# Kernel optimization log

Measured on AMD Instinct MI355X. Metric: run time of the kernel, lower is better.

## Reference

```python
import jax, jax.numpy as jnp
import numpy as np

# Deformable Aggregation (DAF) core of Sparse4DHead1st:
# multi-camera, multi-level bilinear point sampling + grouped weighted reduction.
# feature:            [bs, num_cams, sum(H_l*W_l), C]
# spatial_shapes:     [num_levels, 2] (H, W) per level (static metadata)
# level_start_index:  [num_levels] offsets into the flattened HW axis
# points_2d:          [bs, num_anchor, num_pts, num_cams, 2] normalized (x, y) in [0, 1]
# weights:            [bs, num_anchor, num_pts, num_cams, num_levels, num_groups]
# output:             [bs, num_anchor, C]  (sum over pts, cams, levels)

BS, CAMS, C = 1, 6, 256
NUM_ANCHOR, NUM_PTS = 900, 13
NUM_LEVELS, NUM_GROUPS = 4, 8
LEVEL_SHAPES = np.array([[64, 176], [32, 88], [16, 44], [8, 22]], np.int32)


def setup_inputs() -> dict:
    key = jax.random.key(0)
    k1, k2, k3 = jax.random.split(key, 3)
    hw = LEVEL_SHAPES[:, 0] * LEVEL_SHAPES[:, 1]
    starts = np.concatenate([[0], np.cumsum(hw)[:-1]]).astype(np.int32)
    total = int(hw.sum())  # 14960
    feature = jax.random.normal(k1, (BS, CAMS, total, C), jnp.float32)
    points_2d = jax.random.uniform(k2, (BS, NUM_ANCHOR, NUM_PTS, CAMS, 2), jnp.float32)
    # learned attention weights (normalized-ish so outputs stay O(1))
    weights = jax.random.uniform(
        k3, (BS, NUM_ANCHOR, NUM_PTS, CAMS, NUM_LEVELS, NUM_GROUPS), jnp.float32
    ) / (NUM_PTS * CAMS * NUM_LEVELS)
    return {
        "feature": feature,
        "spatial_shapes": jnp.asarray(LEVEL_SHAPES),
        "level_start_index": jnp.asarray(starts),
        "points_2d": points_2d,
        "weights": weights,
    }


def reference(feature, spatial_shapes, level_start_index, points_2d, weights):
    # spatial shapes / starts are static metadata (control slicing sizes)
    shapes = np.asarray(spatial_shapes)
    starts = np.asarray(level_start_index)
    bs, cams, _, c = feature.shape
    _, A, P, _, _ = points_2d.shape
    L, G = weights.shape[-2], weights.shape[-1]
    gc = c // G  # channels per group
    rowids = jnp.arange(bs * cams)[:, None]

    px = points_2d[..., 0]  # [bs, A, P, cams], normalized x
    py = points_2d[..., 1]

    out = jnp.zeros((bs, A, G, gc), feature.dtype)
    for l in range(L):
        h, w = int(shapes[l, 0]), int(shapes[l, 1])
        s = int(starts[l])
        feat = feature[:, :, s : s + h * w, :].reshape(bs * cams, h * w, c)
        x = px * w - 0.5
        y = py * h - 0.5
        x0 = jnp.floor(x)
        y0 = jnp.floor(y)
        bil = 0.0
        for dx in (0, 1):
            for dy in (0, 1):
                xi = x0 + dx
                yi = y0 + dy
                cw = (1.0 - jnp.abs(x - xi)) * (1.0 - jnp.abs(y - yi))
                valid = (xi >= 0) & (xi < w) & (yi >= 0) & (yi < h)
                idx = (jnp.clip(yi, 0, h - 1) * w + jnp.clip(xi, 0, w - 1)).astype(jnp.int32)
                # [bs, A, P, cams] -> [bs*cams, A*P]
                idx = idx.transpose(0, 3, 1, 2).reshape(bs * cams, A * P)
                cwm = (cw * valid).transpose(0, 3, 1, 2).reshape(bs * cams, A * P)
                v = feat[rowids, idx]  # gather: [bs*cams, A*P, C]
                bil = bil + v * cwm[..., None]
        bil = bil.reshape(bs, cams, A, P, G, gc)
        out = out + jnp.einsum("bcapgd,bapcg->bagd", bil, weights[..., l, :])
    return out.reshape(bs, A, c)
```

## Files before the change

### kernel.cpp

```cpp
#include <hip/hip_runtime.h>

#define NA 900
#define NP 13
#define NCAM 6
#define NL 4
#define NG 8
#define NC 256
#define TOTALHW 14960
#define NPC (NP * NCAM)
#define NS (NPC * NL)
#define NW 8
#define FEAT_ELEMS (NCAM * TOTALHW * NC)

__device__ __constant__ int c_h[NL]  = {64, 32, 16, 8};
__device__ __constant__ int c_w[NL]  = {176, 88, 44, 22};
__device__ __constant__ int c_st[NL] = {0, 11264, 14080, 14784};

__device__ __forceinline__ float bfu(unsigned short u) {
    union { unsigned int i; float f; } x;
    x.i = ((unsigned int)u) << 16;
    return x.f;
}

__global__ __launch_bounds__(256) void cvt_kernel(
    const float* __restrict__ src, unsigned short* __restrict__ dst)
{
    const int n4 = FEAT_ELEMS / 4;
    for (int i = blockIdx.x * 256 + threadIdx.x; i < n4; i += gridDim.x * 256) {
        const float4 v = ((const float4*)src)[i];
        ushort4 o;
        const float* pv = (const float*)&v;
        unsigned short* po = (unsigned short*)&o;
        #pragma unroll
        for (int k = 0; k < 4; ++k) {
            union { float f; unsigned int u; } x;
            x.f = pv[k];
            unsigned int r = x.u + 0x7FFFu + ((x.u >> 16) & 1u);
            po[k] = (unsigned short)(r >> 16);
        }
        ((ushort4*)dst)[i] = o;
    }
}

__global__ __launch_bounds__(512) void daf_bf16_kernel(
    const unsigned short* __restrict__ featb,
    const float* __restrict__ points,
    const float* __restrict__ weights,
    float* __restrict__ out)
{
    const int a    = blockIdx.x;
    const int tid  = threadIdx.x;
    const int wv   = tid >> 6;
    const int lane = tid & 63;

    __shared__ int    s_idx[NS][4];
    __shared__ float  s_cw[NS][4];
    __shared__ float  s_wg[NS * NG];
    __shared__ float4 s_part[NW][64];

    const float* wsrc = weights + (size_t)a * NS * NG;
    for (int i = tid; i < NS * NG; i += 512) {
        const int g  = i & (NG - 1);
        const int s  = i >> 3;
        const int l  = s / NPC;
        const int pc = s - l * NPC;
        s_wg[i] = wsrc[(pc * NL + l) * NG + g];
    }

    if (tid < NS) {
        const int s   = tid;
        const int l   = s / NPC;
        const int pc  = s - l * NPC;
        const int cam = pc % NCAM;
        const int p   = pc / NCAM;

        const float2 pt = *(const float2*)(points + (((size_t)a * NP + p) * NCAM + cam) * 2);
        const int h  = c_h[l];
        const int w  = c_w[l];
        const int st = c_st[l];

        const float x   = pt.x * (float)w - 0.5f;
        const float y   = pt.y * (float)h - 0.5f;
        const float x0f = floorf(x);
        const float y0f = floorf(y);
        const int   x0  = (int)x0f;
        const int   y0  = (int)y0f;
        const float fx  = x - x0f;
        const float fy  = y - y0f;
        const float wx[2] = {1.0f - fx, fx};
        const float wy[2] = {1.0f - fy, fy};

        const int base = cam * TOTALHW + st;
        #pragma unroll
        for (int k = 0; k < 4; ++k) {
            const int dx = k & 1;
            const int dy = k >> 1;
            const int xi = x0 + dx;
            const int yi = y0 + dy;
            const bool valid = (xi >= 0) && (xi < w) && (yi >= 0) && (yi < h);
            const int xc = min(max(xi, 0), w - 1);
            const int yc = min(max(yi, 0), h - 1);
            s_idx[s][k] = base + yc * w + xc;
            s_cw[s][k]  = valid ? wx[dx] * wy[dy] : 0.0f;
        }
    }
    __syncthreads();

    const int g = lane >> 3;
    const ushort4* __restrict__ fb = (const ushort4*)featb;

    float4 acc = make_float4(0.f, 0.f, 0.f, 0.f);
    #pragma unroll 2
    for (int s = wv; s < NS; s += NW) {
        const float wg = s_wg[s * NG + g];
        const int   i0 = s_idx[s][0], i1 = s_idx[s][1], i2 = s_idx[s][2], i3 = s_idx[s][3];
        const float c0 = s_cw[s][0] * wg, c1 = s_cw[s][1] * wg;
        const float c2 = s_cw[s][2] * wg, c3 = s_cw[s][3] * wg;

        const ushort4 r0 = fb[(size_t)i0 * 64 + lane];
        const ushort4 r1 = fb[(size_t)i1 * 64 + lane];
        const ushort4 r2 = fb[(size_t)i2 * 64 + lane];
        const ushort4 r3 = fb[(size_t)i3 * 64 + lane];

        acc.x += bfu(r0.x) * c0 + bfu(r1.x) * c1 + bfu(r2.x) * c2 + bfu(r3.x) * c3;
        acc.y += bfu(r0.y) * c0 + bfu(r1.y) * c1 + bfu(r2.y) * c2 + bfu(r3.y) * c3;
        acc.z += bfu(r0.z) * c0 + bfu(r1.z) * c1 + bfu(r2.z) * c2 + bfu(r3.z) * c3;
        acc.w += bfu(r0.w) * c0 + bfu(r1.w) * c1 + bfu(r2.w) * c2 + bfu(r3.w) * c3;
    }

    s_part[wv][lane] = acc;
    __syncthreads();

    if (tid < 64) {
        float4 r = s_part[0][lane];
        #pragma unroll
        for (int k = 1; k < NW; ++k) {
            const float4 p = s_part[k][lane];
            r.x += p.x; r.y += p.y; r.z += p.z; r.w += p.w;
        }
        ((float4*)out)[(size_t)a * 64 + lane] = r;
    }
}

__global__ __launch_bounds__(512) void daf_f32_kernel(
    const float* __restrict__ feature,
    const float* __restrict__ points,
    const float* __restrict__ weights,
    float* __restrict__ out)
{
    const int a    = blockIdx.x;
    const int tid  = threadIdx.x;
    const int wv   = tid >> 6;
    const int lane = tid & 63;

    __shared__ int    s_idx[NS][4];
    __shared__ float  s_cw[NS][4];
    __shared__ float  s_wg[NS * NG];
    __shared__ float4 s_part[NW][64];

    const float* wsrc = weights + (size_t)a * NS * NG;
    for (int i = tid; i < NS * NG; i += 512) {
        const int g  = i & (NG - 1);
        const int s  = i >> 3;
        const int l  = s / NPC;
        const int pc = s - l * NPC;
        s_wg[i] = wsrc[(pc * NL + l) * NG + g];
    }

    if (tid < NS) {
        const int s   = tid;
        const int l   = s / NPC;
        const int pc  = s - l * NPC;
        const int cam = pc % NCAM;
        const int p   = pc / NCAM;

        const float2 pt = *(const float2*)(points + (((size_t)a * NP + p) * NCAM + cam) * 2);
        const int h  = c_h[l];
        const int w  = c_w[l];
        const int st = c_st[l];

        const float x   = pt.x * (float)w - 0.5f;
        const float y   = pt.y * (float)h - 0.5f;
        const float x0f = floorf(x);
        const float y0f = floorf(y);
        const int   x0  = (int)x0f;
        const int   y0  = (int)y0f;
        const float fx  = x - x0f;
        const float fy  = y - y0f;
        const float wx[2] = {1.0f - fx, fx};
        const float wy[2] = {1.0f - fy, fy};

        const int base = cam * TOTALHW + st;
        #pragma unroll
        for (int k = 0; k < 4; ++k) {
            const int dx = k & 1;
            const int dy = k >> 1;
            const int xi = x0 + dx;
            const int yi = y0 + dy;
            const bool valid = (xi >= 0) && (xi < w) && (yi >= 0) && (yi < h);
            const int xc = min(max(xi, 0), w - 1);
            const int yc = min(max(yi, 0), h - 1);
            s_idx[s][k] = base + yc * w + xc;
            s_cw[s][k]  = valid ? wx[dx] * wy[dy] : 0.0f;
        }
    }
    __syncthreads();

    const int g = lane >> 3;
    const float4* __restrict__ f4 = (const float4*)feature;

    float4 acc = make_float4(0.f, 0.f, 0.f, 0.f);
    for (int s = wv; s < NS; s += NW) {
        const float wg = s_wg[s * NG + g];
        const int   i0 = s_idx[s][0], i1 = s_idx[s][1], i2 = s_idx[s][2], i3 = s_idx[s][3];
        const float c0 = s_cw[s][0] * wg, c1 = s_cw[s][1] * wg;
        const float c2 = s_cw[s][2] * wg, c3 = s_cw[s][3] * wg;

        const float4 v0 = f4[(size_t)i0 * 64 + lane];
        const float4 v1 = f4[(size_t)i1 * 64 + lane];
        const float4 v2 = f4[(size_t)i2 * 64 + lane];
        const float4 v3 = f4[(size_t)i3 * 64 + lane];

        acc.x += v0.x * c0 + v1.x * c1 + v2.x * c2 + v3.x * c3;
        acc.y += v0.y * c0 + v1.y * c1 + v2.y * c2 + v3.y * c3;
        acc.z += v0.z * c0 + v1.z * c1 + v2.z * c2 + v3.z * c3;
        acc.w += v0.w * c0 + v1.w * c1 + v2.w * c2 + v3.w * c3;
    }

    s_part[wv][lane] = acc;
    __syncthreads();

    if (tid < 64) {
        float4 r = s_part[0][lane];
        #pragma unroll
        for (int k = 1; k < NW; ++k) {
            const float4 p = s_part[k][lane];
            r.x += p.x; r.y += p.y; r.z += p.z; r.w += p.w;
        }
        ((float4*)out)[(size_t)a * 64 + lane] = r;
    }
}

extern "C" void kernel_launch(void* const* d_in, const int* in_sizes, int n_in,
                              void* d_out, int out_size, void* d_ws, size_t ws_size,
                              hipStream_t stream) {
    const float* feature        = (const float*)d_in[0];
    const float* points         = (const float*)d_in[3];
    const float* weights        = (const float*)d_in[4];
    float*       out            = (float*)d_out;

    const size_t need = (size_t)FEAT_ELEMS * sizeof(unsigned short);
    if (ws_size >= need && d_ws != nullptr) {
        unsigned short* featb = (unsigned short*)d_ws;
        cvt_kernel<<<2048, 256, 0, stream>>>(feature, featb);
        daf_bf16_kernel<<<NA, 512, 0, stream>>>(featb, points, weights, out);
    } else {
        daf_f32_kernel<<<NA, 512, 0, stream>>>(feature, points, weights, out);
    }
}
```

Before: 204.2 us.

## Split DAF into per-level kernels with software-pipelined gathers and wider bf16 conversion

Replaces the single fused bf16 sampling kernel with four launches, one per pyramid level, each templated on its level shape. Each launch accumulates into the output, and the coarsest level initialises it. Inside each launch the gather loop is software-pipelined: the next sample's four feature rows are prefetched while the current one is accumulated. The conversion kernel now handles eight floats per thread with 16-byte stores. The per-level split is meant to keep one level's feature working set resident in cache, at the cost of three extra launches and read-modify-write traffic on the output.

New measurement: 214.9 us. 1.05x slower.

```diff
diff --git a/kernel.cpp b/kernel.cpp
--- a/kernel.cpp
+++ b/kernel.cpp
@@ -7,14 +7,9 @@
 #define NG 8
 #define NC 256
 #define TOTALHW 14960
-#define NPC (NP * NCAM)
-#define NS (NPC * NL)
 #define NW 8
+#define NSL (NP * NCAM)
 #define FEAT_ELEMS (NCAM * TOTALHW * NC)
-
-__device__ __constant__ int c_h[NL]  = {64, 32, 16, 8};
-__device__ __constant__ int c_w[NL]  = {176, 88, 44, 22};
-__device__ __constant__ int c_st[NL] = {0, 11264, 14080, 14784};
 
 __device__ __forceinline__ float bfu(unsigned short u) {
     union { unsigned int i; float f; } x;
@@ -23,27 +18,162 @@
 }
 
 __global__ __launch_bounds__(256) void cvt_kernel(
-    const float* __restrict__ src, unsigned short* __restrict__ dst)
+    const uint4* __restrict__ src, uint4* __restrict__ dst)
 {
-    const int n4 = FEAT_ELEMS / 4;
-    for (int i = blockIdx.x * 256 + threadIdx.x; i < n4; i += gridDim.x * 256) {
-        const float4 v = ((const float4*)src)[i];
-        ushort4 o;
-        const float* pv = (const float*)&v;
-        unsigned short* po = (unsigned short*)&o;
+    const int n8 = FEAT_ELEMS / 8;
+    for (int i = blockIdx.x * 256 + threadIdx.x; i < n8; i += gridDim.x * 256) {
+        union { uint4 u; float f[4]; } a, b;
+        a.u = src[2 * i];
+        b.u = src[2 * i + 1];
+        unsigned int w[8];
         #pragma unroll
         for (int k = 0; k < 4; ++k) {
             union { float f; unsigned int u; } x;
-            x.f = pv[k];
-            unsigned int r = x.u + 0x7FFFu + ((x.u >> 16) & 1u);
-            po[k] = (unsigned short)(r >> 16);
-        }
-        ((ushort4*)dst)[i] = o;
-    }
-}
-
-__global__ __launch_bounds__(512) void daf_bf16_kernel(
+            x.f = a.f[k];
+            w[k] = (x.u + 0x7FFFu + ((x.u >> 16) & 1u)) >> 16;
+            x.f = b.f[k];
+            w[4 + k] = (x.u + 0x7FFFu + ((x.u >> 16) & 1u)) >> 16;
+        }
+        uint4 o;
+        o.x = w[0] | (w[1] << 16);
+        o.y = w[2] | (w[3] << 16);
+        o.z = w[4] | (w[5] << 16);
+        o.w = w[6] | (w[7] << 16);
+        dst[i] = o;
+    }
+}
+
+template<int L, int H, int W, int ST, bool INIT>
+__global__ __launch_bounds__(512) void daf_level(
     const unsigned short* __restrict__ featb,
+    const float* __restrict__ points,
+    const float* __restrict__ weights,
+    float* __restrict__ out)
+{
+    const int a    = blockIdx.x;
+    const int tid  = threadIdx.x;
+    const int wv   = tid >> 6;
+    const int lane = tid & 63;
+
+    __shared__ int    s_idx[NSL][4];
+    __shared__ float  s_cw[NSL][4];
+    __shared__ float  s_wg[NSL * NG];
+    __shared__ float4 s_part[NW][64];
+
+    const float* wsrc = weights + (size_t)a * NP * NCAM * NL * NG;
+    for (int i = tid; i < NSL * NG; i += 512) {
+        const int g   = i & (NG - 1);
+        const int s   = i >> 3;
+        const int cam = s / NP;
+        const int p   = s - cam * NP;
+        s_wg[i] = wsrc[((p * NCAM + cam) * NL + L) * NG + g];
+    }
+
+    if (tid < NSL) {
+        const int s   = tid;
+        const int cam = s / NP;
+        const int p   = s - cam * NP;
+
+        const float2 pt = *(const float2*)(points + (((size_t)a * NP + p) * NCAM + cam) * 2);
+        const float x   = pt.x * (float)W - 0.5f;
+        const float y   = pt.y * (float)H - 0.5f;
+        const float x0f = floorf(x);
+        const float y0f = floorf(y);
+        const int   x0  = (int)x0f;
+        const int   y0  = (int)y0f;
+        const float fx  = x - x0f;
+        const float fy  = y - y0f;
+        const float wx[2] = {1.0f - fx, fx};
+        const float wy[2] = {1.0f - fy, fy};
+
+        const int base = cam * TOTALHW + ST;
+        #pragma unroll
+        for (int k = 0; k < 4; ++k) {
+            const int dx = k & 1;
+            const int dy = k >> 1;
+            const int xi = x0 + dx;
+            const int yi = y0 + dy;
+            const bool valid = (xi >= 0) && (xi < W) && (yi >= 0) && (yi < H);
+            const int xc = min(max(xi, 0), W - 1);
+            const int yc = min(max(yi, 0), H - 1);
+            s_idx[s][k] = base + yc * W + xc;
+            s_cw[s][k]  = valid ? wx[dx] * wy[dy] : 0.0f;
+        }
+    }
+    __syncthreads();
+
+    const int g = lane >> 3;
+    const ushort4* __restrict__ fb = (const ushort4*)featb;
+
+    float4 acc = make_float4(0.f, 0.f, 0.f, 0.f);
+
+    int s = wv;
+    int4   ii;  float4 cc;  float wg = 0.f;
+    ushort4 r0, r1, r2, r3;
+    if (s < NSL) {
+        ii = *(const int4*)s_idx[s];
+        cc = *(const float4*)s_cw[s];
+        wg = s_wg[s * NG + g];
+        r0 = fb[(size_t)ii.x * 64 + lane];
+        r1 = fb[(size_t)ii.y * 64 + lane];
+        r2 = fb[(size_t)ii.z * 64 + lane];
+        r3 = fb[(size_t)ii.w * 64 + lane];
+    }
+    while (s < NSL) {
+        const int sn = s + NW;
+        int4 ni; float4 nc; float nwg = 0.f;
+        ushort4 n0, n1, n2, n3;
+        if (sn < NSL) {
+            ni  = *(const int4*)s_idx[sn];
+            nc  = *(const float4*)s_cw[sn];
+            nwg = s_wg[sn * NG + g];
+            n0 = fb[(size_t)ni.x * 64 + lane];
+            n1 = fb[(size_t)ni.y * 64 + lane];
+            n2 = fb[(size_t)ni.z * 64 + lane];
+            n3 = fb[(size_t)ni.w * 64 + lane];
+        }
+        const float c0 = cc.x * wg, c1 = cc.y * wg;
+        const float c2 = cc.z * wg, c3 = cc.w * wg;
+
+        acc.x += bfu(r0.x) * c0 + bfu(r1.x) * c1 + bfu(r2.x) * c2 + bfu(r3.x) * c3;
+        acc.y += bfu(r0.y) * c0 + bfu(r1.y) * c1 + bfu(r2.y) * c2 + bfu(r3.y) * c3;
+        acc.z += bfu(r0.z) * c0 + bfu(r1.z) * c1 + bfu(r2.z) * c2 + bfu(r3.z) * c3;
+        acc.w += bfu(r0.w) * c0 + bfu(r1.w) * c1 + bfu(r2.w) * c2 + bfu(r3.w) * c3;
+
+        r0 = n0; r1 = n1; r2 = n2; r3 = n3;
+        cc = nc; wg = nwg;
+        s = sn;
+    }
+
+    s_part[wv][lane] = acc;
+    __syncthreads();
+
+    if (tid < 64) {
+        float4 r = s_part[0][lane];
+        #pragma unroll
+        for (int k = 1; k < NW; ++k) {
+            const float4 p = s_part[k][lane];
+            r.x += p.x; r.y += p.y; r.z += p.z; r.w += p.w;
+        }
+        float4* po = (float4*)out + (size_t)a * 64 + lane;
+        if (INIT) {
+            *po = r;
+        } else {
+            float4 t = *po;
+            t.x += r.x; t.y += r.y; t.z += r.z; t.w += r.w;
+            *po = t;
+        }
+    }
+}
+
+#define NPC (NP * NCAM)
+#define NS (NPC * NL)
+__device__ __constant__ int c_h[NL]  = {64, 32, 16, 8};
+__device__ __constant__ int c_w[NL]  = {176, 88, 44, 22};
+__device__ __constant__ int c_st[NL] = {0, 11264, 14080, 14784};
+
+__global__ __launch_bounds__(512) void daf_f32_kernel(
+    const float* __restrict__ feature,
     const float* __restrict__ points,
     const float* __restrict__ weights,
     float* __restrict__ out)
@@ -107,106 +237,6 @@
     __syncthreads();
 
     const int g = lane >> 3;
-    const ushort4* __restrict__ fb = (const ushort4*)featb;
-
-    float4 acc = make_float4(0.f, 0.f, 0.f, 0.f);
-    #pragma unroll 2
-    for (int s = wv; s < NS; s += NW) {
-        const float wg = s_wg[s * NG + g];
-        const int   i0 = s_idx[s][0], i1 = s_idx[s][1], i2 = s_idx[s][2], i3 = s_idx[s][3];
-        const float c0 = s_cw[s][0] * wg, c1 = s_cw[s][1] * wg;
-        const float c2 = s_cw[s][2] * wg, c3 = s_cw[s][3] * wg;
-
-        const ushort4 r0 = fb[(size_t)i0 * 64 + lane];
-        const ushort4 r1 = fb[(size_t)i1 * 64 + lane];
-        const ushort4 r2 = fb[(size_t)i2 * 64 + lane];
-        const ushort4 r3 = fb[(size_t)i3 * 64 + lane];
-
-        acc.x += bfu(r0.x) * c0 + bfu(r1.x) * c1 + bfu(r2.x) * c2 + bfu(r3.x) * c3;
-        acc.y += bfu(r0.y) * c0 + bfu(r1.y) * c1 + bfu(r2.y) * c2 + bfu(r3.y) * c3;
-        acc.z += bfu(r0.z) * c0 + bfu(r1.z) * c1 + bfu(r2.z) * c2 + bfu(r3.z) * c3;
-        acc.w += bfu(r0.w) * c0 + bfu(r1.w) * c1 + bfu(r2.w) * c2 + bfu(r3.w) * c3;
-    }
-
-    s_part[wv][lane] = acc;
-    __syncthreads();
-
-    if (tid < 64) {
-        float4 r = s_part[0][lane];
-        #pragma unroll
-        for (int k = 1; k < NW; ++k) {
-            const float4 p = s_part[k][lane];
-            r.x += p.x; r.y += p.y; r.z += p.z; r.w += p.w;
-        }
-        ((float4*)out)[(size_t)a * 64 + lane] = r;
-    }
-}
-
-__global__ __launch_bounds__(512) void daf_f32_kernel(
-    const float* __restrict__ feature,
-    const float* __restrict__ points,
-    const float* __restrict__ weights,
-    float* __restrict__ out)
-{
-    const int a    = blockIdx.x;
-    const int tid  = threadIdx.x;
-    const int wv   = tid >> 6;
-    const int lane = tid & 63;
-
-    __shared__ int    s_idx[NS][4];
-    __shared__ float  s_cw[NS][4];
-    __shared__ float  s_wg[NS * NG];
-    __shared__ float4 s_part[NW][64];
-
-    const float* wsrc = weights + (size_t)a * NS * NG;
-    for (int i = tid; i < NS * NG; i += 512) {
-        const int g  = i & (NG - 1);
-        const int s  = i >> 3;
-        const int l  = s / NPC;
-        const int pc = s - l * NPC;
-        s_wg[i] = wsrc[(pc * NL + l) * NG + g];
-    }
-
-    if (tid < NS) {
-        const int s   = tid;
-        const int l   = s / NPC;
-        const int pc  = s - l * NPC;
-        const int cam = pc % NCAM;
-        const int p   = pc / NCAM;
-
-        const float2 pt = *(const float2*)(points + (((size_t)a * NP + p) * NCAM + cam) * 2);
-        const int h  = c_h[l];
-        const int w  = c_w[l];
-        const int st = c_st[l];
-
-        const float x   = pt.x * (float)w - 0.5f;
-        const float y   = pt.y * (float)h - 0.5f;
-        const float x0f = floorf(x);
-        const float y0f = floorf(y);
-        const int   x0  = (int)x0f;
-        const int   y0  = (int)y0f;
-        const float fx  = x - x0f;
-        const float fy  = y - y0f;
-        const float wx[2] = {1.0f - fx, fx};
-        const float wy[2] = {1.0f - fy, fy};
-
-        const int base = cam * TOTALHW + st;
-        #pragma unroll
-        for (int k = 0; k < 4; ++k) {
-            const int dx = k & 1;
-            const int dy = k >> 1;
-            const int xi = x0 + dx;
-            const int yi = y0 + dy;
-            const bool valid = (xi >= 0) && (xi < w) && (yi >= 0) && (yi < h);
-            const int xc = min(max(xi, 0), w - 1);
-            const int yc = min(max(yi, 0), h - 1);
-            s_idx[s][k] = base + yc * w + xc;
-            s_cw[s][k]  = valid ? wx[dx] * wy[dy] : 0.0f;
-        }
-    }
-    __syncthreads();
-
-    const int g = lane >> 3;
     const float4* __restrict__ f4 = (const float4*)feature;
 
     float4 acc = make_float4(0.f, 0.f, 0.f, 0.f);
@@ -244,16 +274,19 @@
 extern "C" void kernel_launch(void* const* d_in, const int* in_sizes, int n_in,
                               void* d_out, int out_size, void* d_ws, size_t ws_size,
                               hipStream_t stream) {
-    const float* feature        = (const float*)d_in[0];
-    const float* points         = (const float*)d_in[3];
-    const float* weights        = (const float*)d_in[4];
-    float*       out            = (float*)d_out;
+    const float* feature = (const float*)d_in[0];
+    const float* points  = (const float*)d_in[3];
+    const float* weights = (const float*)d_in[4];
+    float*       out     = (float*)d_out;
 
     const size_t need = (size_t)FEAT_ELEMS * sizeof(unsigned short);
     if (ws_size >= need && d_ws != nullptr) {
         unsigned short* featb = (unsigned short*)d_ws;
-        cvt_kernel<<<2048, 256, 0, stream>>>(feature, featb);
-        daf_bf16_kernel<<<NA, 512, 0, stream>>>(featb, points, weights, out);
+        cvt_kernel<<<2048, 256, 0, stream>>>((const uint4*)feature, (uint4*)featb);
+        daf_level<3,  8,  22, 14784, true ><<<NA, 512, 0, stream>>>(featb, points, weights, out);
+        daf_level<2, 16,  44, 14080, false><<<NA, 512, 0, stream>>>(featb, points, weights, out);
+        daf_level<1, 32,  88, 11264, false><<<NA, 512, 0, stream>>>(featb, points, weights, out);
+        daf_level<0, 64, 176,     0, false><<<NA, 512, 0, stream>>>(featb, points, weights, out);
     } else {
         daf_f32_kernel<<<NA, 512, 0, stream>>>(feature, points, weights, out);
     }
```
